# Kernel optimization log

Measured on AMD Instinct MI355X. Metric: run time of the kernel, lower is better.

The kernel has to match this reference:

```python
import jax, jax.numpy as jnp
import numpy as np

N = 100_000   # nodes
E = 1_600_000 # edges
D = 128       # hidden/input dim
OUT = 32      # output dim
G = 512       # graphs in batch
L = 3         # conv layers


def setup_inputs() -> dict:
    key = jax.random.key(0)
    ks = jax.random.split(key, 12)
    s = 1.0 / np.sqrt(D)
    inp = {
        "x": jax.random.normal(ks[0], (N, D), jnp.float32),
        "edge_index": jax.random.randint(ks[1], (2, E), 0, N, dtype=jnp.int32),
        "batch": jnp.sort(jax.random.randint(ks[2], (N,), 0, G, dtype=jnp.int32)),
        "enc_W1": jax.random.normal(ks[3], (D, D), jnp.float32) * s,
        "enc_b1": jnp.zeros((D,), jnp.float32),
        "enc_W2": jax.random.normal(ks[4], (D, D), jnp.float32) * s,
        "enc_b2": jnp.zeros((D,), jnp.float32),
        "gcn_W": jax.random.normal(ks[5], (L, D, D), jnp.float32) * s,
        "gcn_b": jnp.zeros((L, D), jnp.float32),
        "dec_W1": jax.random.normal(ks[6], (D, D), jnp.float32) * s,
        "dec_b1": jnp.zeros((D,), jnp.float32),
        "dec_W2": jax.random.normal(ks[7], (D, OUT), jnp.float32) * s,
        "dec_b2": jnp.zeros((OUT,), jnp.float32),
        "num_graphs": G,
    }
    return inp


def reference(x, edge_index, batch, enc_W1, enc_b1, enc_W2, enc_b2,
              gcn_W, gcn_b, dec_W1, dec_b1, dec_W2, dec_b2, num_graphs):
    n = x.shape[0]
    src, dst = edge_index[0], edge_index[1]

    # ---- encoder MLP (Linear -> ReLU -> Linear -> ReLU) ----
    h = jax.nn.relu(x @ enc_W1 + enc_b1)
    h = jax.nn.relu(h @ enc_W2 + enc_b2)

    # ---- GCN normalization: D^{-1/2} (A + I) D^{-1/2}, degrees incl. self-loops ----
    deg = jax.ops.segment_sum(jnp.ones_like(src, dtype=h.dtype), dst, num_segments=n) + 1.0
    inv_sqrt = jax.lax.rsqrt(deg)           # [N]
    edge_coef = inv_sqrt[src] * inv_sqrt[dst]  # [E]
    self_coef = inv_sqrt * inv_sqrt            # [N]

    # ---- GCN conv layers ----
    for l in range(gcn_W.shape[0]):
        hw = h @ gcn_W[l]                                       # [N, D]
        msgs = hw[src] * edge_coef[:, None]                     # [E, D] gather
        agg = jax.ops.segment_sum(msgs, dst, num_segments=n)    # [N, D] scatter-add
        agg = agg + hw * self_coef[:, None]                     # self loops
        h = jax.nn.relu(agg + gcn_b[l])

    # ---- global add pool over graphs ----
    pooled = jax.ops.segment_sum(h, batch, num_segments=num_graphs)  # [G, D]

    # ---- decoder MLP ----
    out = jax.nn.relu(pooled @ dec_W1 + dec_b1)
    return out @ dec_W2 + dec_b2
```

## Files before the change

kernel.cpp:

```cpp
#include <hip/hip_runtime.h>

#define NNODES 100000
#define NEDGES 1600000
#define DIM    128
#define OUTD   32
#define NGRAPH 512

#define NBUCK2  256
#define BSHIFT  9
#define CAP     12288
#define EPB2    8192
#define SBLOCKS ((NEDGES + EPB2 - 1) / EPB2)
#define NBUILD  ((NNODES + 511) / 512)
#define EBLOCKS ((NNODES + 63) / 64)
#define AGGBLK  ((NNODES + 31) / 32)

using bf16x8 = __attribute__((ext_vector_type(8))) short;
using f32x4  = __attribute__((ext_vector_type(4))) float;
using f32x2  = __attribute__((ext_vector_type(2))) float;

__device__ __forceinline__ short f2bf(float f) {
    unsigned u = __float_as_uint(f);
    unsigned r = (u + 0x7fff + ((u >> 16) & 1)) >> 16;
    return (short)r;
}
__device__ __forceinline__ float bf2f(short s) {
    return __uint_as_float(((unsigned)(unsigned short)s) << 16);
}

__device__ __forceinline__ uint2 bf8_to_fp8(bf16x8 t) {
    float f0 = bf2f(t[0]), f1 = bf2f(t[1]), f2 = bf2f(t[2]), f3 = bf2f(t[3]);
    float f4 = bf2f(t[4]), f5 = bf2f(t[5]), f6 = bf2f(t[6]), f7 = bf2f(t[7]);
    uint2 o;
    o.x = __builtin_amdgcn_cvt_pk_fp8_f32(f0, f1, 0, false);
    o.x = __builtin_amdgcn_cvt_pk_fp8_f32(f2, f3, o.x, true);
    o.y = __builtin_amdgcn_cvt_pk_fp8_f32(f4, f5, 0, false);
    o.y = __builtin_amdgcn_cvt_pk_fp8_f32(f6, f7, o.y, true);
    return o;
}

__global__ __launch_bounds__(256) void k_prep(
    const float* __restrict__ eW1, const float* __restrict__ eW2,
    const float* __restrict__ gW, short* __restrict__ WT,
    int* __restrict__ gcur, float* __restrict__ pooled)
{
    int idx = blockIdx.x * 256 + threadIdx.x;
    if (idx < 5 * 16384) {
        int mat = idx >> 14, rem = idx & 16383;
        int k = rem >> 7, n = rem & 127;
        const float* src = (mat == 0) ? eW1 : (mat == 1) ? eW2
                                            : (gW + (size_t)(mat - 2) * 16384);
        WT[(size_t)mat * 16384 + n * DIM + k] = f2bf(src[k * DIM + n]);
    }
    if (idx < NBUCK2) gcur[idx] = idx * CAP;
    if (idx < NGRAPH * DIM) pooled[idx] = 0.f;
}

__global__ __launch_bounds__(512) void k_scatter(
    const int* __restrict__ src, const int* __restrict__ dst,
    int* __restrict__ gcur, unsigned* __restrict__ tmp)
{
    __shared__ unsigned short rnk[EPB2];
    __shared__ int h[NBUCK2];
    __shared__ int gbase[NBUCK2];
    const int tid  = threadIdx.x;
    const int base = blockIdx.x * EPB2;
    if (tid < NBUCK2) h[tid] = 0;
    __syncthreads();
    #pragma unroll
    for (int it = 0; it < EPB2 / 512; ++it) {
        int e = base + it * 512 + tid;
        if (e < NEDGES) {
            int b = dst[e] >> BSHIFT;
            rnk[it * 512 + tid] = (unsigned short)atomicAdd(&h[b], 1);
        }
    }
    __syncthreads();
    if (tid < NBUCK2 && h[tid] > 0)
        gbase[tid] = atomicAdd(&gcur[tid], h[tid]);
    __syncthreads();
    #pragma unroll
    for (int it = 0; it < EPB2 / 512; ++it) {
        int e = base + it * 512 + tid;
        if (e < NEDGES) {
            int d = dst[e], sv = src[e];
            int b = d >> BSHIFT;
            int pos = gbase[b] + rnk[it * 512 + tid];
            if (pos < (b + 1) * CAP)
                tmp[pos] = (unsigned)sv | ((unsigned)(d & 511) << 17);
        }
    }
}

__global__ __launch_bounds__(512) void k_build(
    const unsigned* __restrict__ tmp, const int* __restrict__ gcur,
    int* __restrict__ row_off, int* __restrict__ cntA,
    float* __restrict__ inv, int* __restrict__ col)
{
    __shared__ int hist[512], sc[512], lcur[512];
    const int tid   = threadIdx.x;
    const int b     = blockIdx.x;
    const int tbase = b * CAP;
    const int cnt_b = min(gcur[b] - tbase, CAP);
    hist[tid] = 0;
    __syncthreads();
    for (int i = tid; i < cnt_b; i += 512)
        atomicAdd(&hist[(tmp[tbase + i] >> 17) & 511], 1);
    __syncthreads();
    const int hv = hist[tid];
    sc[tid] = hv;
    __syncthreads();
    for (int off = 1; off < 512; off <<= 1) {
        int t = (tid >= off) ? sc[tid - off] : 0;
        __syncthreads();
        sc[tid] += t;
        __syncthreads();
    }
    const int start = tbase + sc[tid] - hv;
    lcur[tid] = start;
    const int node = b * 512 + tid;
    if (node < NNODES) {
        row_off[node] = start;
        cntA[node]    = hv;
        inv[node]     = rsqrtf((float)hv + 1.0f);
    }
    __syncthreads();
    for (int i = tid; i < cnt_b; i += 512) {
        unsigned t = tmp[tbase + i];
        int pos = atomicAdd(&lcur[(t >> 17) & 511], 1);
        col[pos] = (int)((t & 0x1FFFFu) << 7);
    }
}

__global__ __launch_bounds__(512, 6) void k_enc(
    const float* __restrict__ x, const short* __restrict__ WT,
    const float* __restrict__ b1, const float* __restrict__ b2,
    const float* __restrict__ inv, unsigned char* __restrict__ g8, int M)
{
    __shared__ short As[64 * 128];
    __shared__ short Bs[128 * 128];

    const int tid = threadIdx.x;
    const int m0  = blockIdx.x * 64;

    #pragma unroll
    for (int i = 0; i < 2; ++i) {
        int u = tid + i * 512;
        int row = u >> 4, c = u & 15;
        int gr = min(m0 + row, M - 1);
        const float4* sp = (const float4*)(x + (size_t)gr * DIM + (c << 3));
        float4 f0 = sp[0], f1 = sp[1];
        short t8[8] = { f2bf(f0.x), f2bf(f0.y), f2bf(f0.z), f2bf(f0.w),
                        f2bf(f1.x), f2bf(f1.y), f2bf(f1.z), f2bf(f1.w) };
        *(bf16x8*)&As[row * 128 + ((c ^ (row & 15)) << 3)] = *(bf16x8*)t8;
    }

    const int wave = tid >> 6, lane = tid & 63;
    const int ml = lane & 15, quad = lane >> 4;
    const int rw = wave >> 1;
    const int cw = wave & 1;

    #pragma unroll
    for (int mat = 0; mat < 3; ++mat) {
        if (mat > 0) __syncthreads();
        #pragma unroll
        for (int i = 0; i < 4; ++i) {
            int u = tid + i * 512;
            int n = u >> 4, c = u & 15;
            *(bf16x8*)&Bs[n * 128 + ((c ^ (n & 15)) << 3)] =
                *(const bf16x8*)(WT + (size_t)mat * 16384 + n * DIM + (c << 3));
        }
        __syncthreads();

        f32x4 acc[4] = {};
        const int arow = rw * 16 + ml;
        #pragma unroll
        for (int kk = 0; kk < 4; ++kk) {
            const int c = kk * 4 + quad;
            bf16x8 a = *(bf16x8*)&As[arow * 128 + ((c ^ (arow & 15)) << 3)];
            #pragma unroll
            for (int ni = 0; ni < 4; ++ni) {
                const int brow = (cw * 4 + ni) * 16 + ml;
                bf16x8 b = *(bf16x8*)&Bs[brow * 128 + ((c ^ (brow & 15)) << 3)];
                acc[ni] = __builtin_amdgcn_mfma_f32_16x16x32_bf16(a, b, acc[ni], 0, 0, 0);
            }
        }
        __syncthreads();

        #pragma unroll
        for (int ni = 0; ni < 4; ++ni) {
            const int colc = cw * 64 + ni * 16 + ml;
            const int cc = colc >> 3, w = colc & 7;
            #pragma unroll
            for (int r = 0; r < 4; ++r) {
                const int rowl = rw * 16 + quad * 4 + r;
                float v = acc[ni][r];
                if (mat == 0)      v = fmaxf(v + b1[colc], 0.f);
                else if (mat == 1) v = fmaxf(v + b2[colc], 0.f);
                else               v *= inv[min(m0 + rowl, M - 1)];
                As[rowl * 128 + (((cc ^ (rowl & 15)) << 3) | w)] = f2bf(v);
            }
        }
    }
    __syncthreads();

    #pragma unroll
    for (int i = 0; i < 2; ++i) {
        int u = tid + i * 512;
        int row = u >> 4, c = u & 15;
        int gr = m0 + row;
        if (gr < M) {
            bf16x8 t = *(bf16x8*)&As[row * 128 + ((c ^ (row & 15)) << 3)];
            *(uint2*)(g8 + (size_t)gr * DIM + (c << 3)) = bf8_to_fp8(t);
        }
    }
}

__global__ __launch_bounds__(512, 8) void k_agg_gemm(
    const unsigned char* __restrict__ g8v, const int* __restrict__ row_off,
    const int* __restrict__ cntA, const int* __restrict__ col,
    const float* __restrict__ inv, const float* __restrict__ bias,
    const short* __restrict__ WT, unsigned char* __restrict__ g8o)
{
    __shared__ short As[32 * 128];
    __shared__ short Bs[128 * 128];

    const int tid = threadIdx.x;

    #pragma unroll
    for (int i = 0; i < 4; ++i) {
        int u = tid + i * 512;
        int n = u >> 4, c = u & 15;
        *(bf16x8*)&Bs[n * 128 + ((c ^ (n & 15)) << 3)] =
            *(const bf16x8*)(WT + n * DIM + (c << 3));
    }

    const int wave = tid >> 6, lane = tid & 63;
    const int q    = lane >> 4;
    const int sl   = lane & 15;
    const int sl8  = sl << 3;
    const int nl   = wave * 4 + q;
    const int m0   = blockIdx.x * 32;
    const int node = m0 + nl;

    f32x2 a01, a23, a45, a67;
    {
        uint2 us = *(const uint2*)(g8v + (size_t)node * 128 + sl8);
        a01 = __builtin_amdgcn_cvt_pk_f32_fp8(us.x, false);
        a23 = __builtin_amdgcn_cvt_pk_f32_fp8(us.x, true);
        a45 = __builtin_amdgcn_cvt_pk_f32_fp8(us.y, false);
        a67 = __builtin_amdgcn_cvt_pk_f32_fp8(us.y, true);
    }

    #define ACC8(v) \
        a01 += __builtin_amdgcn_cvt_pk_f32_fp8(v.x, false); \
        a23 += __builtin_amdgcn_cvt_pk_f32_fp8(v.x, true);  \
        a45 += __builtin_amdgcn_cvt_pk_f32_fp8(v.y, false); \
        a67 += __builtin_amdgcn_cvt_pk_f32_fp8(v.y, true);
    #define GLD(c) (*(const uint2*)(g8v + (size_t)(unsigned)((c) + sl8)))

    const int s = row_off[node];
    const int e = s + cntA[node];
    int j = s;
    for (; j + 7 < e; j += 8) {
        uint2 v0 = GLD(col[j]);
        uint2 v1 = GLD(col[j + 1]);
        uint2 v2 = GLD(col[j + 2]);
        uint2 v3 = GLD(col[j + 3]);
        uint2 v4 = GLD(col[j + 4]);
        uint2 v5 = GLD(col[j + 5]);
        uint2 v6 = GLD(col[j + 6]);
        uint2 v7 = GLD(col[j + 7]);
        ACC8(v0) ACC8(v1) ACC8(v2) ACC8(v3)
        ACC8(v4) ACC8(v5) ACC8(v6) ACC8(v7)
    }
    for (; j + 3 < e; j += 4) {
        uint2 v0 = GLD(col[j]);
        uint2 v1 = GLD(col[j + 1]);
        uint2 v2 = GLD(col[j + 2]);
        uint2 v3 = GLD(col[j + 3]);
        ACC8(v0) ACC8(v1) ACC8(v2) ACC8(v3)
    }
    for (; j < e; ++j) {
        uint2 v = GLD(col[j]);
        ACC8(v)
    }
    #undef ACC8
    #undef GLD

    const float scv = inv[node];
    const float4 bb0 = ((const float4*)bias)[sl * 2];
    const float4 bb1 = ((const float4*)bias)[sl * 2 + 1];
    short o[8];
    o[0] = f2bf(fmaxf(fmaf(a01[0], scv, bb0.x), 0.f));
    o[1] = f2bf(fmaxf(fmaf(a01[1], scv, bb0.y), 0.f));
    o[2] = f2bf(fmaxf(fmaf(a23[0], scv, bb0.z), 0.f));
    o[3] = f2bf(fmaxf(fmaf(a23[1], scv, bb0.w), 0.f));
    o[4] = f2bf(fmaxf(fmaf(a45[0], scv, bb1.x), 0.f));
    o[5] = f2bf(fmaxf(fmaf(a45[1], scv, bb1.y), 0.f));
    o[6] = f2bf(fmaxf(fmaf(a67[0], scv, bb1.z), 0.f));
    o[7] = f2bf(fmaxf(fmaf(a67[1], scv, bb1.w), 0.f));
    *(bf16x8*)&As[nl * 128 + ((sl ^ (nl & 15)) << 3)] = *(bf16x8*)o;
    __syncthreads();

    const int mh = wave >> 2;
    const int nq = wave & 3;
    f32x4 acc[2] = {};
    #pragma unroll
    for (int kk = 0; kk < 4; ++kk) {
        const int c = kk * 4 + q;
        bf16x8 a = *(bf16x8*)&As[(mh * 16 + sl) * 128 + ((c ^ sl) << 3)];
        #pragma unroll
        for (int ni = 0; ni < 2; ++ni) {
            bf16x8 b = *(bf16x8*)&Bs[((nq * 2 + ni) * 16 + sl) * 128 + ((c ^ sl) << 3)];
            acc[ni] = __builtin_amdgcn_mfma_f32_16x16x32_bf16(a, b, acc[ni], 0, 0, 0);
        }
    }
    __syncthreads();

    #pragma unroll
    for (int ni = 0; ni < 2; ++ni) {
        const int colc = (nq * 2 + ni) * 16 + sl;
        const int cc   = colc >> 3, cw = colc & 7;
        #pragma unroll
        for (int r = 0; r < 4; ++r) {
            const int rowl = mh * 16 + q * 4 + r;
            As[rowl * 128 + (((cc ^ (rowl & 15)) << 3) | cw)] =
                f2bf(acc[ni][r] * inv[m0 + rowl]);
        }
    }
    __syncthreads();

    {
        int row = tid >> 4, c = tid & 15;
        bf16x8 t = *(bf16x8*)&As[row * 128 + ((c ^ (row & 15)) << 3)];
        *(uint2*)(g8o + (size_t)(m0 + row) * DIM + (c << 3)) = bf8_to_fp8(t);
    }
}

__global__ __launch_bounds__(512) void k_agg_pool(
    const unsigned char* __restrict__ g8v, const int* __restrict__ row_off,
    const int* __restrict__ cntA, const int* __restrict__ col,
    const float* __restrict__ inv, const float* __restrict__ bias,
    const int* __restrict__ batch, float* __restrict__ pooled)
{
    __shared__ float Hs[32][132];
    __shared__ int sbatch[32];

    const int tid = threadIdx.x;
    const int wave = tid >> 6, lane = tid & 63;
    const int q    = lane >> 4;
    const int sl   = lane & 15;
    const int sl8  = sl << 3;
    const int nl   = wave * 4 + q;
    const int m0   = blockIdx.x * 32;
    const int node = m0 + nl;

    if (tid < 32) sbatch[tid] = batch[m0 + tid];

    f32x2 a01, a23, a45, a67;
    {
        uint2 us = *(const uint2*)(g8v + (size_t)node * 128 + sl8);
        a01 = __builtin_amdgcn_cvt_pk_f32_fp8(us.x, false);
        a23 = __builtin_amdgcn_cvt_pk_f32_fp8(us.x, true);
        a45 = __builtin_amdgcn_cvt_pk_f32_fp8(us.y, false);
        a67 = __builtin_amdgcn_cvt_pk_f32_fp8(us.y, true);
    }

    #define ACC8(v) \
        a01 += __builtin_amdgcn_cvt_pk_f32_fp8(v.x, false); \
        a23 += __builtin_amdgcn_cvt_pk_f32_fp8(v.x, true);  \
        a45 += __builtin_amdgcn_cvt_pk_f32_fp8(v.y, false); \
        a67 += __builtin_amdgcn_cvt_pk_f32_fp8(v.y, true);
    #define GLD(c) (*(const uint2*)(g8v + (size_t)(unsigned)((c) + sl8)))

    const int s = row_off[node];
    const int e = s + cntA[node];
    int j = s;
    for (; j + 7 < e; j += 8) {
        uint2 v0 = GLD(col[j]);
        uint2 v1 = GLD(col[j + 1]);
        uint2 v2 = GLD(col[j + 2]);
        uint2 v3 = GLD(col[j + 3]);
        uint2 v4 = GLD(col[j + 4]);
        uint2 v5 = GLD(col[j + 5]);
        uint2 v6 = GLD(col[j + 6]);
        uint2 v7 = GLD(col[j + 7]);
        ACC8(v0) ACC8(v1) ACC8(v2) ACC8(v3)
        ACC8(v4) ACC8(v5) ACC8(v6) ACC8(v7)
    }
    for (; j + 3 < e; j += 4) {
        uint2 v0 = GLD(col[j]);
        uint2 v1 = GLD(col[j + 1]);
        uint2 v2 = GLD(col[j + 2]);
        uint2 v3 = GLD(col[j + 3]);
        ACC8(v0) ACC8(v1) ACC8(v2) ACC8(v3)
    }
    for (; j < e; ++j) {
        uint2 v = GLD(col[j]);
        ACC8(v)
    }
    #undef ACC8
    #undef GLD

    const float scv = inv[node];
    const float4 bb0 = ((const float4*)bias)[sl * 2];
    const float4 bb1 = ((const float4*)bias)[sl * 2 + 1];
    float4 h0, h1;
    h0.x = fmaxf(fmaf(a01[0], scv, bb0.x), 0.f);
    h0.y = fmaxf(fmaf(a01[1], scv, bb0.y), 0.f);
    h0.z = fmaxf(fmaf(a23[0], scv, bb0.z), 0.f);
    h0.w = fmaxf(fmaf(a23[1], scv, bb0.w), 0.f);
    h1.x = fmaxf(fmaf(a45[0], scv, bb1.x), 0.f);
    h1.y = fmaxf(fmaf(a45[1], scv, bb1.y), 0.f);
    h1.z = fmaxf(fmaf(a67[0], scv, bb1.z), 0.f);
    h1.w = fmaxf(fmaf(a67[1], scv, bb1.w), 0.f);
    *(float4*)&Hs[nl][sl * 8]     = h0;
    *(float4*)&Hs[nl][sl * 8 + 4] = h1;
    __syncthreads();

    const int d   = tid & 127;
    const int grp = tid >> 7;
    float acc = 0.f;
    int cg = -1;
    #pragma unroll
    for (int i = 0; i < 8; ++i) {
        const int nn = grp * 8 + i;
        const int g  = sbatch[nn];
        if (g != cg) {
            if (cg >= 0) atomicAdd(pooled + (size_t)cg * DIM + d, acc);
            cg = g; acc = 0.f;
        }
        acc += Hs[nn][d];
    }
    atomicAdd(pooled + (size_t)cg * DIM + d, acc);
}

__global__ __launch_bounds__(512) void k_dec(
    const float* __restrict__ pooled, const float* __restrict__ W1,
    const float* __restrict__ b1, const float* __restrict__ W2,
    const float* __restrict__ b2, float* __restrict__ out)
{
    __shared__ float pbuf[8][128];
    __shared__ float tbuf[8][128];
    const int wave = threadIdx.x >> 6, lane = threadIdx.x & 63;
    const int g = blockIdx.x * 8 + wave;

    float2 pv = *(const float2*)(pooled + (size_t)g * DIM + lane * 2);
    pbuf[wave][lane * 2]     = pv.x;
    pbuf[wave][lane * 2 + 1] = pv.y;
    __syncthreads();

    float t0 = 0.f, t1 = 0.f;
    #pragma unroll 8
    for (int k = 0; k < DIM; ++k) {
        float pk = pbuf[wave][k];
        float2 w = *(const float2*)(W1 + (size_t)k * DIM + lane * 2);
        t0 = fmaf(pk, w.x, t0);
        t1 = fmaf(pk, w.y, t1);
    }
    tbuf[wave][lane * 2]     = fmaxf(t0 + b1[lane * 2],     0.f);
    tbuf[wave][lane * 2 + 1] = fmaxf(t1 + b1[lane * 2 + 1], 0.f);
    __syncthreads();

    const int c = lane & 31, hh = lane >> 5;
    float part = 0.f;
    #pragma unroll 8
    for (int kk = 0; kk < 64; ++kk) {
        int k = hh * 64 + kk;
        part = fmaf(tbuf[wave][k], W2[(size_t)k * OUTD + c], part);
    }
    float other = __shfl_xor(part, 32, 64);
    if (hh == 0)
        out[(size_t)g * OUTD + c] = part + other + b2[c];
}

extern "C" void kernel_launch(void* const* d_in, const int* in_sizes, int n_in,
                              void* d_out, int out_size, void* d_ws, size_t ws_size,
                              hipStream_t stream)
{
    const float* x      = (const float*)d_in[0];
    const int*   ei     = (const int*)d_in[1];
    const int*   batch  = (const int*)d_in[2];
    const float* enc_W1 = (const float*)d_in[3];
    const float* enc_b1 = (const float*)d_in[4];
    const float* enc_W2 = (const float*)d_in[5];
    const float* enc_b2 = (const float*)d_in[6];
    const float* gcn_W  = (const float*)d_in[7];
    const float* gcn_b  = (const float*)d_in[8];
    const float* dec_W1 = (const float*)d_in[9];
    const float* dec_b1 = (const float*)d_in[10];
    const float* dec_W2 = (const float*)d_in[11];
    const float* dec_b2 = (const float*)d_in[12];
    float* out = (float*)d_out;

    const int* src = ei;
    const int* dst = ei + NEDGES;

    char* p = (char*)d_ws;
    auto alloc = [&](size_t bytes) -> void* {
        void* r = (void*)p;
        p += (bytes + 255) & ~(size_t)255;
        return r;
    };
    unsigned char* g8a    = (unsigned char*)alloc((size_t)NNODES * DIM);
    unsigned char* g8b    = (unsigned char*)alloc((size_t)NNODES * DIM);
    float*         inv    = (float*)        alloc((size_t)NNODES * sizeof(float));
    int*           row_off= (int*)          alloc((size_t)NNODES * sizeof(int));
    int*           cntA   = (int*)          alloc((size_t)NNODES * sizeof(int));
    int*           col    = (int*)          alloc((size_t)NBUCK2 * CAP * sizeof(int));
    unsigned*      tmp    = (unsigned*)     alloc((size_t)NBUCK2 * CAP * sizeof(unsigned));
    int*           gcur   = (int*)          alloc((size_t)NBUCK2 * sizeof(int));
    short*         WT     = (short*)        alloc((size_t)5 * DIM * DIM * sizeof(short));
    float*         pooled = (float*)        alloc((size_t)NGRAPH * DIM * sizeof(float));

    k_prep   <<<(5 * 16384 + 255) / 256, 256, 0, stream>>>(enc_W1, enc_W2, gcn_W,
                                                           WT, gcur, pooled);
    k_scatter<<<SBLOCKS, 512, 0, stream>>>(src, dst, gcur, tmp);
    k_build  <<<NBUILD, 512, 0, stream>>>(tmp, gcur, row_off, cntA, inv, col);

    k_enc<<<EBLOCKS, 512, 0, stream>>>(x, WT, enc_b1, enc_b2, inv, g8a, NNODES);

    k_agg_gemm<<<AGGBLK, 512, 0, stream>>>(g8a, row_off, cntA, col, inv,
                                           gcn_b,       WT + 3 * 16384, g8b);
    k_agg_gemm<<<AGGBLK, 512, 0, stream>>>(g8b, row_off, cntA, col, inv,
                                           gcn_b + 128, WT + 4 * 16384, g8a);
    k_agg_pool<<<AGGBLK, 512, 0, stream>>>(g8a, row_off, cntA, col, inv,
                                           gcn_b + 256, batch, pooled);

    k_dec <<<NGRAPH / 8, 512, 0, stream>>>(pooled, dec_W1, dec_b1,
                                           dec_W2, dec_b2, out);
}
```

Baseline: 292.9 us.

## Build CSR with global atomic degree count and fill; software-pipeline neighbor gathers

New measurement: 442.2 us. 51.0% more time.

```diff
diff --git a/kernel.cpp b/kernel.cpp
--- a/kernel.cpp
+++ b/kernel.cpp
@@ -7,13 +7,11 @@
 #define NGRAPH 512
 
 #define NBUCK2  256
-#define BSHIFT  9
 #define CAP     12288
-#define EPB2    8192
-#define SBLOCKS ((NEDGES + EPB2 - 1) / EPB2)
 #define NBUILD  ((NNODES + 511) / 512)
 #define EBLOCKS ((NNODES + 63) / 64)
 #define AGGBLK  ((NNODES + 31) / 32)
+#define TBLOCKS ((NEDGES + 511) / 512)
 
 using bf16x8 = __attribute__((ext_vector_type(8))) short;
 using f32x4  = __attribute__((ext_vector_type(4))) float;
@@ -42,7 +40,7 @@
 __global__ __launch_bounds__(256) void k_prep(
     const float* __restrict__ eW1, const float* __restrict__ eW2,
     const float* __restrict__ gW, short* __restrict__ WT,
-    int* __restrict__ gcur, float* __restrict__ pooled)
+    int* __restrict__ deg, float* __restrict__ pooled)
 {
     int idx = blockIdx.x * 256 + threadIdx.x;
     if (idx < 5 * 16384) {
@@ -52,83 +50,51 @@
                                             : (gW + (size_t)(mat - 2) * 16384);
         WT[(size_t)mat * 16384 + n * DIM + k] = f2bf(src[k * DIM + n]);
     }
-    if (idx < NBUCK2) gcur[idx] = idx * CAP;
+    if (idx < NNODES) deg[idx] = 0;
     if (idx < NGRAPH * DIM) pooled[idx] = 0.f;
 }
 
-__global__ __launch_bounds__(512) void k_scatter(
-    const int* __restrict__ src, const int* __restrict__ dst,
-    int* __restrict__ gcur, unsigned* __restrict__ tmp)
-{
-    __shared__ unsigned short rnk[EPB2];
-    __shared__ int h[NBUCK2];
-    __shared__ int gbase[NBUCK2];
-    const int tid  = threadIdx.x;
-    const int base = blockIdx.x * EPB2;
-    if (tid < NBUCK2) h[tid] = 0;
-    __syncthreads();
-    #pragma unroll
-    for (int it = 0; it < EPB2 / 512; ++it) {
-        int e = base + it * 512 + tid;
-        if (e < NEDGES) {
-            int b = dst[e] >> BSHIFT;
-            rnk[it * 512 + tid] = (unsigned short)atomicAdd(&h[b], 1);
-        }
-    }
-    __syncthreads();
-    if (tid < NBUCK2 && h[tid] > 0)
-        gbase[tid] = atomicAdd(&gcur[tid], h[tid]);
-    __syncthreads();
-    #pragma unroll
-    for (int it = 0; it < EPB2 / 512; ++it) {
-        int e = base + it * 512 + tid;
-        if (e < NEDGES) {
-            int d = dst[e], sv = src[e];
-            int b = d >> BSHIFT;
-            int pos = gbase[b] + rnk[it * 512 + tid];
-            if (pos < (b + 1) * CAP)
-                tmp[pos] = (unsigned)sv | ((unsigned)(d & 511) << 17);
-        }
-    }
-}
-
-__global__ __launch_bounds__(512) void k_build(
-    const unsigned* __restrict__ tmp, const int* __restrict__ gcur,
-    int* __restrict__ row_off, int* __restrict__ cntA,
-    float* __restrict__ inv, int* __restrict__ col)
-{
-    __shared__ int hist[512], sc[512], lcur[512];
-    const int tid   = threadIdx.x;
-    const int b     = blockIdx.x;
-    const int tbase = b * CAP;
-    const int cnt_b = min(gcur[b] - tbase, CAP);
-    hist[tid] = 0;
-    __syncthreads();
-    for (int i = tid; i < cnt_b; i += 512)
-        atomicAdd(&hist[(tmp[tbase + i] >> 17) & 511], 1);
-    __syncthreads();
-    const int hv = hist[tid];
-    sc[tid] = hv;
+__global__ __launch_bounds__(512) void k_deg(
+    const int* __restrict__ dst, int* __restrict__ deg)
+{
+    int e = blockIdx.x * 512 + threadIdx.x;
+    if (e < NEDGES) atomicAdd(&deg[dst[e]], 1);
+}
+
+__global__ __launch_bounds__(512) void k_scan(
+    const int* __restrict__ deg, int* __restrict__ row_off,
+    int* __restrict__ cur, float* __restrict__ inv)
+{
+    __shared__ int sc[512];
+    const int b = blockIdx.x, t = threadIdx.x;
+    const int node = b * 512 + t;
+    const int d = (node < NNODES) ? deg[node] : 0;
+    sc[t] = d;
     __syncthreads();
     for (int off = 1; off < 512; off <<= 1) {
-        int t = (tid >= off) ? sc[tid - off] : 0;
+        int v = (t >= off) ? sc[t - off] : 0;
         __syncthreads();
-        sc[tid] += t;
+        sc[t] += v;
         __syncthreads();
     }
-    const int start = tbase + sc[tid] - hv;
-    lcur[tid] = start;
-    const int node = b * 512 + tid;
+    const int start = b * CAP + sc[t] - d;
     if (node < NNODES) {
         row_off[node] = start;
-        cntA[node]    = hv;
-        inv[node]     = rsqrtf((float)hv + 1.0f);
-    }
-    __syncthreads();
-    for (int i = tid; i < cnt_b; i += 512) {
-        unsigned t = tmp[tbase + i];
-        int pos = atomicAdd(&lcur[(t >> 17) & 511], 1);
-        col[pos] = (int)((t & 0x1FFFFu) << 7);
+        cur[node]     = start;
+        inv[node]     = rsqrtf((float)d + 1.0f);
+    }
+}
+
+__global__ __launch_bounds__(512) void k_fill(
+    const int* __restrict__ src, const int* __restrict__ dst,
+    int* __restrict__ cur, int* __restrict__ col)
+{
+    int e = blockIdx.x * 512 + threadIdx.x;
+    if (e < NEDGES) {
+        int d = dst[e];
+        int pos = atomicAdd(&cur[d], 1);
+        if (pos < ((d >> 9) + 1) * CAP)
+            col[pos] = src[e] << 7;
     }
 }
 
@@ -216,6 +182,45 @@
     }
 }
 
+#define GATHER_PIPELINE(GBASE)                                                 \
+    const int s = row_off[node];                                               \
+    const int e = s + cntA[node];                                              \
+    int j = s;                                                                 \
+    {                                                                          \
+        uint2 b0, b1_, b2_, b3_, b4_, b5_, b6_, b7_;                           \
+        const bool hav = (j + 7 < e);                                          \
+        if (hav) {                                                             \
+            b0 = GLD(col[j]);     b1_ = GLD(col[j + 1]);                       \
+            b2_ = GLD(col[j + 2]); b3_ = GLD(col[j + 3]);                      \
+            b4_ = GLD(col[j + 4]); b5_ = GLD(col[j + 5]);                      \
+            b6_ = GLD(col[j + 6]); b7_ = GLD(col[j + 7]);                      \
+            j += 8;                                                            \
+        }                                                                      \
+        for (; j + 7 < e; j += 8) {                                            \
+            uint2 n0 = GLD(col[j]);     uint2 n1 = GLD(col[j + 1]);            \
+            uint2 n2 = GLD(col[j + 2]); uint2 n3 = GLD(col[j + 3]);            \
+            uint2 n4 = GLD(col[j + 4]); uint2 n5 = GLD(col[j + 5]);            \
+            uint2 n6 = GLD(col[j + 6]); uint2 n7 = GLD(col[j + 7]);            \
+            ACC8(b0) ACC8(b1_) ACC8(b2_) ACC8(b3_)                             \
+            ACC8(b4_) ACC8(b5_) ACC8(b6_) ACC8(b7_)                            \
+            b0 = n0; b1_ = n1; b2_ = n2; b3_ = n3;                             \
+            b4_ = n4; b5_ = n5; b6_ = n6; b7_ = n7;                            \
+        }                                                                      \
+        if (hav) {                                                             \
+            ACC8(b0) ACC8(b1_) ACC8(b2_) ACC8(b3_)                             \
+            ACC8(b4_) ACC8(b5_) ACC8(b6_) ACC8(b7_)                            \
+        }                                                                      \
+    }                                                                          \
+    for (; j + 3 < e; j += 4) {                                                \
+        uint2 v0 = GLD(col[j]);     uint2 v1 = GLD(col[j + 1]);                \
+        uint2 v2 = GLD(col[j + 2]); uint2 v3 = GLD(col[j + 3]);                \
+        ACC8(v0) ACC8(v1) ACC8(v2) ACC8(v3)                                    \
+    }                                                                          \
+    for (; j < e; ++j) {                                                       \
+        uint2 v = GLD(col[j]);                                                 \
+        ACC8(v)                                                                \
+    }
+
 __global__ __launch_bounds__(512, 8) void k_agg_gemm(
     const unsigned char* __restrict__ g8v, const int* __restrict__ row_off,
     const int* __restrict__ cntA, const int* __restrict__ col,
@@ -259,32 +264,8 @@
         a67 += __builtin_amdgcn_cvt_pk_f32_fp8(v.y, true);
     #define GLD(c) (*(const uint2*)(g8v + (size_t)(unsigned)((c) + sl8)))
 
-    const int s = row_off[node];
-    const int e = s + cntA[node];
-    int j = s;
-    for (; j + 7 < e; j += 8) {
-        uint2 v0 = GLD(col[j]);
-        uint2 v1 = GLD(col[j + 1]);
-        uint2 v2 = GLD(col[j + 2]);
-        uint2 v3 = GLD(col[j + 3]);
-        uint2 v4 = GLD(col[j + 4]);
-        uint2 v5 = GLD(col[j + 5]);
-        uint2 v6 = GLD(col[j + 6]);
-        uint2 v7 = GLD(col[j + 7]);
-        ACC8(v0) ACC8(v1) ACC8(v2) ACC8(v3)
-        ACC8(v4) ACC8(v5) ACC8(v6) ACC8(v7)
-    }
-    for (; j + 3 < e; j += 4) {
-        uint2 v0 = GLD(col[j]);
-        uint2 v1 = GLD(col[j + 1]);
-        uint2 v2 = GLD(col[j + 2]);
-        uint2 v3 = GLD(col[j + 3]);
-        ACC8(v0) ACC8(v1) ACC8(v2) ACC8(v3)
-    }
-    for (; j < e; ++j) {
-        uint2 v = GLD(col[j]);
-        ACC8(v)
-    }
+    GATHER_PIPELINE(g8v)
+
     #undef ACC8
     #undef GLD
 
@@ -374,32 +355,8 @@
         a67 += __builtin_amdgcn_cvt_pk_f32_fp8(v.y, true);
     #define GLD(c) (*(const uint2*)(g8v + (size_t)(unsigned)((c) + sl8)))
 
-    const int s = row_off[node];
-    const int e = s + cntA[node];
-    int j = s;
-    for (; j + 7 < e; j += 8) {
-        uint2 v0 = GLD(col[j]);
-        uint2 v1 = GLD(col[j + 1]);
-        uint2 v2 = GLD(col[j + 2]);
-        uint2 v3 = GLD(col[j + 3]);
-        uint2 v4 = GLD(col[j + 4]);
-        uint2 v5 = GLD(col[j + 5]);
-        uint2 v6 = GLD(col[j + 6]);
-        uint2 v7 = GLD(col[j + 7]);
-        ACC8(v0) ACC8(v1) ACC8(v2) ACC8(v3)
-        ACC8(v4) ACC8(v5) ACC8(v6) ACC8(v7)
-    }
-    for (; j + 3 < e; j += 4) {
-        uint2 v0 = GLD(col[j]);
-        uint2 v1 = GLD(col[j + 1]);
-        uint2 v2 = GLD(col[j + 2]);
-        uint2 v3 = GLD(col[j + 3]);
-        ACC8(v0) ACC8(v1) ACC8(v2) ACC8(v3)
-    }
-    for (; j < e; ++j) {
-        uint2 v = GLD(col[j]);
-        ACC8(v)
-    }
+    GATHER_PIPELINE(g8v)
+
     #undef ACC8
     #undef GLD
 
@@ -507,25 +464,25 @@
     unsigned char* g8b    = (unsigned char*)alloc((size_t)NNODES * DIM);
     float*         inv    = (float*)        alloc((size_t)NNODES * sizeof(float));
     int*           row_off= (int*)          alloc((size_t)NNODES * sizeof(int));
-    int*           cntA   = (int*)          alloc((size_t)NNODES * sizeof(int));
+    int*           deg    = (int*)          alloc((size_t)NNODES * sizeof(int));
+    int*           cur    = (int*)          alloc((size_t)NNODES * sizeof(int));
     int*           col    = (int*)          alloc((size_t)NBUCK2 * CAP * sizeof(int));
-    unsigned*      tmp    = (unsigned*)     alloc((size_t)NBUCK2 * CAP * sizeof(unsigned));
-    int*           gcur   = (int*)          alloc((size_t)NBUCK2 * sizeof(int));
     short*         WT     = (short*)        alloc((size_t)5 * DIM * DIM * sizeof(short));
     float*         pooled = (float*)        alloc((size_t)NGRAPH * DIM * sizeof(float));
 
-    k_prep   <<<(5 * 16384 + 255) / 256, 256, 0, stream>>>(enc_W1, enc_W2, gcn_W,
-                                                           WT, gcur, pooled);
-    k_scatter<<<SBLOCKS, 512, 0, stream>>>(src, dst, gcur, tmp);
-    k_build  <<<NBUILD, 512, 0, stream>>>(tmp, gcur, row_off, cntA, inv, col);
+    k_prep <<<(NNODES + 255) / 256, 256, 0, stream>>>(enc_W1, enc_W2, gcn_W,
+                                                      WT, deg, pooled);
+    k_deg  <<<TBLOCKS, 512, 0, stream>>>(dst, deg);
+    k_scan <<<NBUILD, 512, 0, stream>>>(deg, row_off, cur, inv);
+    k_fill <<<TBLOCKS, 512, 0, stream>>>(src, dst, cur, col);
 
     k_enc<<<EBLOCKS, 512, 0, stream>>>(x, WT, enc_b1, enc_b2, inv, g8a, NNODES);
 
-    k_agg_gemm<<<AGGBLK, 512, 0, stream>>>(g8a, row_off, cntA, col, inv,
+    k_agg_gemm<<<AGGBLK, 512, 0, stream>>>(g8a, row_off, deg, col, inv,
                                            gcn_b,       WT + 3 * 16384, g8b);
-    k_agg_gemm<<<AGGBLK, 512, 0, stream>>>(g8b, row_off, cntA, col, inv,
+    k_agg_gemm<<<AGGBLK, 512, 0, stream>>>(g8b, row_off, deg, col, inv,
                                            gcn_b + 128, WT + 4 * 16384, g8a);
-    k_agg_pool<<<AGGBLK, 512, 0, stream>>>(g8a, row_off, cntA, col, inv,
+    k_agg_pool<<<AGGBLK, 512, 0, stream>>>(g8a, row_off, deg, col, inv,
                                            gcn_b + 256, batch, pooled);
 
     k_dec <<<NGRAPH / 8, 512, 0, stream>>>(pooled, dec_W1, dec_b1,
```
